# Kernel optimization log

Measured on AMD Instinct MI355X. Metric: run time of the kernel, lower is better.

Reference implementation:

```python
import jax, jax.numpy as jnp
import numpy as np

WEIGHT_MSE = 1.0 / 3.0
W_DNA, W_RNA, W_LIG = 5.0, 5.0, 10.0
EPS = 1e-6


def _weighted_rigid_align(x, x_target, w):
    # x, x_target: [..., N, 3]; w: [..., N]. Aligns x onto x_target (Kabsch).
    w3 = w[..., None]                                   # [..., N, 1]
    wsum = jnp.sum(w, axis=-1, keepdims=True)[..., None]  # [..., 1, 1]
    mu_x = jnp.sum(w3 * x, axis=-2, keepdims=True) / wsum
    mu_t = jnp.sum(w3 * x_target, axis=-2, keepdims=True) / wsum
    xc = x - mu_x
    tc = x_target - mu_t
    # weighted covariance H = sum_n w_n * tc_n tc? -> [..., 3, 3]
    H = jnp.einsum('...ni,...nj->...ij', w3 * tc, xc)
    U, _, Vt = jnp.linalg.svd(H)
    d = jnp.sign(jnp.linalg.det(U @ Vt))                # reflection fix
    D = jnp.stack([jnp.ones_like(d), jnp.ones_like(d), d], axis=-1)
    R = (U * D[..., None, :]) @ Vt                      # [..., 3, 3]
    return jnp.einsum('...ij,...nj->...ni', R, xc) + mu_t


def setup_inputs() -> dict:
    key = jax.random.key(0)
    ks = jax.random.split(key, 7)
    B, S, N = 8, 48, 8192
    pred = jax.random.normal(ks[0], (B, S, N, 3), dtype=jnp.float32)
    true = jax.random.normal(ks[1], (B, N, 3), dtype=jnp.float32)
    mask = jax.random.randint(ks[2], (B, N), 0, 2, dtype=jnp.int32)
    is_dna = jax.random.randint(ks[3], (B, N), 0, 2, dtype=jnp.int32)
    is_rna = jax.random.randint(ks[4], (B, N), 0, 2, dtype=jnp.int32)
    is_lig = jax.random.randint(ks[5], (B, N), 0, 2, dtype=jnp.int32)
    scale = jax.random.uniform(ks[6], (B, S), dtype=jnp.float32)
    return {"pred_coordinate": pred, "true_coordinate": true,
            "coordinate_mask": mask, "is_dna": is_dna, "is_rna": is_rna,
            "is_ligand": is_lig, "per_sample_scale": scale}


def reference(pred_coordinate, true_coordinate, coordinate_mask, is_dna,
              is_rna, is_ligand, per_sample_scale):
    S = pred_coordinate.shape[-3]
    mask = coordinate_mask.astype(jnp.float32)          # [B, N]
    weight = (1.0 + W_DNA * is_dna.astype(jnp.float32)
              + W_RNA * is_rna.astype(jnp.float32)
              + W_LIG * is_ligand.astype(jnp.float32)) * mask
    true_m = true_coordinate * mask[..., None]          # [B, N, 3]
    pred_m = pred_coordinate * mask[..., None, :, None]  # [B, S, N, 3]
    true_e = jnp.broadcast_to(true_m[..., None, :, :], pred_coordinate.shape)
    weight_e = jnp.broadcast_to(weight[..., None, :],
                                pred_coordinate.shape[:-1])  # [B, S, N]
    aligned = jax.lax.stop_gradient(
        _weighted_rigid_align(true_e, pred_m, weight_e))
    weight_e = jax.lax.stop_gradient(weight_e)
    per_atom_se = jnp.sum((pred_coordinate - aligned) ** 2, axis=-1)  # [B,S,N]
    denom = jnp.sum(mask, axis=-1, keepdims=True) + EPS               # [B,1]
    per_sample = jnp.sum(weight_e * per_atom_se, axis=-1) / denom     # [B,S]
    per_sample = per_sample * per_sample_scale
    loss_b = WEIGHT_MSE * jnp.mean(per_sample, axis=-1)               # [B]
    return jnp.mean(loss_b)
```

## Files before the change

### kernel.cpp

```cpp
#include <hip/hip_runtime.h>
#include <math.h>

namespace {

constexpr int NB = 8;
constexpr int NS = 48;
constexpr int NA = 8192;
constexpr int BSIZE = 256;
constexpr int CH = 4;
constexpr int NBS = NB * NS;
constexpr int GRID = CH * NBS;
constexpr int FBS = NBS;

constexpr int PBOFF = NBS * CH * 16;

template <int CNT>
__device__ inline void blockReduceWrite(const float (&v)[CNT], float* __restrict__ dst,
                                        float* lds) {
  const int lane = threadIdx.x & 63;
  const int wave = threadIdx.x >> 6;
#pragma unroll
  for (int k = 0; k < CNT; ++k) {
    float x = v[k];
#pragma unroll
    for (int off = 32; off; off >>= 1) x += __shfl_xor(x, off, 64);
    if (lane == 0) lds[wave * CNT + k] = x;
  }
  __syncthreads();
  if ((int)threadIdx.x < CNT) {
    float s = 0.f;
#pragma unroll
    for (int w = 0; w < BSIZE / 64; ++w) s += lds[w * CNT + threadIdx.x];
    dst[threadIdx.x] = s;
  }
  __syncthreads();
}

__global__ __launch_bounds__(BSIZE) void fused_kernel(
    const float* __restrict__ pred, const float* __restrict__ truec,
    const int* __restrict__ mask, const int* __restrict__ dna,
    const int* __restrict__ rna, const int* __restrict__ lig,
    float* __restrict__ ws) {
  __shared__ float lds[(BSIZE / 64) * 13];
  const int blk = blockIdx.x;
  const int c = blk / NBS;
  const int bs = blk % NBS;
  const int b = bs / NS;
  const bool isS0 = (bs % NS) == 0;

  const float* p = pred + (size_t)bs * NA * 3;
  const float* t = truec + (size_t)b * NA * 3;
  const int mbase = b * NA;

  float acc[13];
#pragma unroll
  for (int k = 0; k < 13; ++k) acc[k] = 0.f;
  float accb[6];
#pragma unroll
  for (int k = 0; k < 6; ++k) accb[k] = 0.f;

  auto atom = [&](float w, float p0, float p1, float p2, float t0, float t1, float t2) {
    const float wp0 = w * p0, wp1 = w * p1, wp2 = w * p2;
    acc[0] += wp0 * p0 + wp1 * p1 + wp2 * p2;
    acc[1] += wp0;
    acc[2] += wp1;
    acc[3] += wp2;
    acc[4] += wp0 * t0;
    acc[5] += wp0 * t1;
    acc[6] += wp0 * t2;
    acc[7] += wp1 * t0;
    acc[8] += wp1 * t1;
    acc[9] += wp1 * t2;
    acc[10] += wp2 * t0;
    acc[11] += wp2 * t1;
    acc[12] += wp2 * t2;
  };
  auto atomb = [&](float mf, float w, float t0, float t1, float t2) {
    accb[0] += w;
    accb[1] += w * t0;
    accb[2] += w * t1;
    accb[3] += w * t2;
    accb[4] += w * (t0 * t0 + t1 * t1 + t2 * t2);
    accb[5] += mf;
  };
  auto wgt = [](int m, int d, int r, int l) {
    return (float)((1 + 5 * (d + r) + 10 * l) * m);
  };

#pragma unroll
  for (int it = 0; it < 2; ++it) {
    const int n0 = c * 2048 + it * 1024 + threadIdx.x * 4;
    const float4 pa = *(const float4*)(p + 3 * n0);
    const float4 pb = *(const float4*)(p + 3 * n0 + 4);
    const float4 pc = *(const float4*)(p + 3 * n0 + 8);
    const float4 ta = *(const float4*)(t + 3 * n0);
    const float4 tb = *(const float4*)(t + 3 * n0 + 4);
    const float4 tc = *(const float4*)(t + 3 * n0 + 8);
    const int4 mk = *(const int4*)(mask + mbase + n0);
    const int4 dn = *(const int4*)(dna + mbase + n0);
    const int4 rn = *(const int4*)(rna + mbase + n0);
    const int4 lg = *(const int4*)(lig + mbase + n0);

    const float w0 = wgt(mk.x, dn.x, rn.x, lg.x);
    const float w1 = wgt(mk.y, dn.y, rn.y, lg.y);
    const float w2 = wgt(mk.z, dn.z, rn.z, lg.z);
    const float w3 = wgt(mk.w, dn.w, rn.w, lg.w);

    atom(w0, pa.x, pa.y, pa.z, ta.x, ta.y, ta.z);
    atom(w1, pa.w, pb.x, pb.y, ta.w, tb.x, tb.y);
    atom(w2, pb.z, pb.w, pc.x, tb.z, tb.w, tc.x);
    atom(w3, pc.y, pc.z, pc.w, tc.y, tc.z, tc.w);

    if (isS0) {
      atomb((float)mk.x, w0, ta.x, ta.y, ta.z);
      atomb((float)mk.y, w1, ta.w, tb.x, tb.y);
      atomb((float)mk.z, w2, tb.z, tb.w, tc.x);
      atomb((float)mk.w, w3, tc.y, tc.z, tc.w);
    }
  }

  blockReduceWrite<13>(acc, ws + (size_t)(bs * CH + c) * 16, lds);
  if (isS0) blockReduceWrite<6>(accb, ws + PBOFF + (size_t)(b * CH + c) * 8, lds);
}

__global__ __launch_bounds__(FBS) void final_kernel(const float* __restrict__ ws,
                                                    const float* __restrict__ scale,
                                                    float* __restrict__ out) {
  const int tid = threadIdx.x;
  __shared__ double bv[NB][6];

  if (tid < NB) {
    double s[6] = {0, 0, 0, 0, 0, 0};
    for (int c = 0; c < CH; ++c) {
      const float* q = ws + PBOFF + (tid * CH + c) * 8;
#pragma unroll
      for (int k = 0; k < 6; ++k) s[k] += (double)q[k];
    }
#pragma unroll
    for (int k = 0; k < 6; ++k) bv[tid][k] = s[k];
  }
  __syncthreads();

  const int b = tid / NS;
  double sums[13];
#pragma unroll
  for (int k = 0; k < 13; ++k) sums[k] = 0.0;
  for (int c = 0; c < CH; ++c) {
    const float4* q4 = (const float4*)(ws + (size_t)(tid * CH + c) * 16);
    const float4 qa = q4[0], qb = q4[1], qc = q4[2], qd = q4[3];
    sums[0] += (double)qa.x;  sums[1] += (double)qa.y;
    sums[2] += (double)qa.z;  sums[3] += (double)qa.w;
    sums[4] += (double)qb.x;  sums[5] += (double)qb.y;
    sums[6] += (double)qb.z;  sums[7] += (double)qb.w;
    sums[8] += (double)qc.x;  sums[9] += (double)qc.y;
    sums[10] += (double)qc.z; sums[11] += (double)qc.w;
    sums[12] += (double)qd.x;
  }

  const double wsum = bv[b][0];
  const double St[3] = {bv[b][1], bv[b][2], bv[b][3]};
  const double stt = bv[b][4];
  const double msum = bv[b][5];

  const double spp = sums[0];
  const double Sp[3] = {sums[1], sums[2], sums[3]};
  const double inv = 1.0 / wsum;

  double H[3][3];
#pragma unroll
  for (int i = 0; i < 3; ++i)
#pragma unroll
    for (int j = 0; j < 3; ++j) H[i][j] = sums[4 + 3 * i + j] - Sp[i] * St[j] * inv;

  const double Sq = spp - (Sp[0] * Sp[0] + Sp[1] * Sp[1] + Sp[2] * Sp[2]) * inv;
  const double Sy = stt - (St[0] * St[0] + St[1] * St[1] + St[2] * St[2]) * inv;

  double K[3][3];
#pragma unroll
  for (int i = 0; i < 3; ++i)
#pragma unroll
    for (int j = 0; j < 3; ++j)
      K[i][j] = H[0][i] * H[0][j] + H[1][i] * H[1][j] + H[2][i] * H[2][j];

  const double q = (K[0][0] + K[1][1] + K[2][2]) / 3.0;
  const double p1 = K[0][1] * K[0][1] + K[0][2] * K[0][2] + K[1][2] * K[1][2];
  const double a0 = K[0][0] - q, a1 = K[1][1] - q, a2 = K[2][2] - q;
  const double p2 = a0 * a0 + a1 * a1 + a2 * a2 + 2.0 * p1;
  double e1, e2, e3;
  if (p2 <= 1e-300) {
    e1 = e2 = e3 = q;
  } else {
    const double pp = sqrt(p2 / 6.0);
    const double ip = 1.0 / pp;
    const double B00 = a0 * ip, B11 = a1 * ip, B22 = a2 * ip;
    const double B01 = K[0][1] * ip, B02 = K[0][2] * ip, B12 = K[1][2] * ip;
    double r = 0.5 * (B00 * (B11 * B22 - B12 * B12) - B01 * (B01 * B22 - B12 * B02) +
                      B02 * (B01 * B12 - B11 * B02));
    float rf = fminf(1.0f, fmaxf(-1.0f, (float)r));
    const float phi = acosf(rf) * (1.0f / 3.0f);
    e1 = q + 2.0 * pp * (double)cosf(phi);
    e3 = q + 2.0 * pp * (double)cosf(phi + 2.0943951023931953f);
    e2 = 3.0 * q - e1 - e3;
  }
  const double s1 = sqrt(fmax(e1, 0.0));
  const double s2 = sqrt(fmax(e2, 0.0));
  const double s3 = sqrt(fmax(e3, 0.0));

  const double detH =
      H[0][0] * (H[1][1] * H[2][2] - H[1][2] * H[2][1]) -
      H[0][1] * (H[1][0] * H[2][2] - H[1][2] * H[2][0]) +
      H[0][2] * (H[1][0] * H[2][1] - H[1][1] * H[2][0]);
  const double d = (detH > 0.0) ? 1.0 : ((detH < 0.0) ? -1.0 : 0.0);

  const double cost = Sq + Sy - 2.0 * (s1 + s2 + d * s3);
  double tot = cost / (msum + 1e-6) * (double)scale[tid];
  tot *= 1.0 / (3.0 * (double)NS * (double)NB);

#pragma unroll
  for (int off = 32; off; off >>= 1) tot += __shfl_xor(tot, off, 64);
  __shared__ double red[FBS / 64];
  if ((tid & 63) == 0) red[tid >> 6] = tot;
  __syncthreads();
  if (tid == 0) {
    double s = 0.0;
#pragma unroll
    for (int w = 0; w < FBS / 64; ++w) s += red[w];
    out[0] = (float)s;
  }
}

}

extern "C" void kernel_launch(void* const* d_in, const int* in_sizes, int n_in,
                              void* d_out, int out_size, void* d_ws, size_t ws_size,
                              hipStream_t stream) {
  const float* pred = (const float*)d_in[0];
  const float* truec = (const float*)d_in[1];
  const int* mask = (const int*)d_in[2];
  const int* dna = (const int*)d_in[3];
  const int* rna = (const int*)d_in[4];
  const int* lig = (const int*)d_in[5];
  const float* scale = (const float*)d_in[6];
  float* ws = (float*)d_ws;
  float* out = (float*)d_out;

  fused_kernel<<<GRID, BSIZE, 0, stream>>>(pred, truec, mask, dna, rna, lig, ws);
  final_kernel<<<1, FBS, 0, stream>>>(ws, scale, out);
}
```

Measured before the change: 25.04 us.

## Fuse partial reduction and Kabsch finalization into one kernel with atomic output

Replaces the two-kernel design (chunked partial sums plus a single-block final kernel) with one kernel where each 512-thread block handles a whole (batch, sample) pair, computes the per-batch true-coordinate statistics itself, solves the 3x3 alignment cost in thread 0, and atomically adds its contribution to the output after a memset. This removes the second launch and the workspace round trip. In exchange it gives up chunk-level parallelism (384 blocks instead of 1536), recomputes the per-batch statistics in every sample block, and makes the final sum depend on float atomic ordering.

Measured after the change: 35.37 us. 41.2% more time.

```diff
diff --git a/kernel.cpp b/kernel.cpp
--- a/kernel.cpp
+++ b/kernel.cpp
@@ -6,48 +6,18 @@
 constexpr int NB = 8;
 constexpr int NS = 48;
 constexpr int NA = 8192;
-constexpr int BSIZE = 256;
-constexpr int CH = 4;
+constexpr int TPB = 512;
 constexpr int NBS = NB * NS;
-constexpr int GRID = CH * NBS;
-constexpr int FBS = NBS;
+constexpr int NW = TPB / 64;
 
-constexpr int PBOFF = NBS * CH * 16;
 
-template <int CNT>
-__device__ inline void blockReduceWrite(const float (&v)[CNT], float* __restrict__ dst,
-                                        float* lds) {
-  const int lane = threadIdx.x & 63;
-  const int wave = threadIdx.x >> 6;
-#pragma unroll
-  for (int k = 0; k < CNT; ++k) {
-    float x = v[k];
-#pragma unroll
-    for (int off = 32; off; off >>= 1) x += __shfl_xor(x, off, 64);
-    if (lane == 0) lds[wave * CNT + k] = x;
-  }
-  __syncthreads();
-  if ((int)threadIdx.x < CNT) {
-    float s = 0.f;
-#pragma unroll
-    for (int w = 0; w < BSIZE / 64; ++w) s += lds[w * CNT + threadIdx.x];
-    dst[threadIdx.x] = s;
-  }
-  __syncthreads();
-}
-
-__global__ __launch_bounds__(BSIZE) void fused_kernel(
+__global__ __launch_bounds__(TPB, 4) void loss_kernel(
     const float* __restrict__ pred, const float* __restrict__ truec,
     const int* __restrict__ mask, const int* __restrict__ dna,
     const int* __restrict__ rna, const int* __restrict__ lig,
-    float* __restrict__ ws) {
-  __shared__ float lds[(BSIZE / 64) * 13];
-  const int blk = blockIdx.x;
-  const int c = blk / NBS;
-  const int bs = blk % NBS;
+    const float* __restrict__ scale, float* __restrict__ out) {
+  const int bs = blockIdx.x;
   const int b = bs / NS;
-  const bool isS0 = (bs % NS) == 0;
-
   const float* p = pred + (size_t)bs * NA * 3;
   const float* t = truec + (size_t)b * NA * 3;
   const int mbase = b * NA;
@@ -59,7 +29,8 @@
 #pragma unroll
   for (int k = 0; k < 6; ++k) accb[k] = 0.f;
 
-  auto atom = [&](float w, float p0, float p1, float p2, float t0, float t1, float t2) {
+  auto atom = [&](float mf, float w, float p0, float p1, float p2, float t0,
+                  float t1, float t2) {
     const float wp0 = w * p0, wp1 = w * p1, wp2 = w * p2;
     acc[0] += wp0 * p0 + wp1 * p1 + wp2 * p2;
     acc[1] += wp0;
@@ -74,8 +45,6 @@
     acc[10] += wp2 * t0;
     acc[11] += wp2 * t1;
     acc[12] += wp2 * t2;
-  };
-  auto atomb = [&](float mf, float w, float t0, float t1, float t2) {
     accb[0] += w;
     accb[1] += w * t0;
     accb[2] += w * t1;
@@ -88,8 +57,8 @@
   };
 
 #pragma unroll
-  for (int it = 0; it < 2; ++it) {
-    const int n0 = c * 2048 + it * 1024 + threadIdx.x * 4;
+  for (int it = 0; it < NA / (TPB * 4); ++it) {
+    const int n0 = it * (TPB * 4) + threadIdx.x * 4;
     const float4 pa = *(const float4*)(p + 3 * n0);
     const float4 pb = *(const float4*)(p + 3 * n0 + 4);
     const float4 pc = *(const float4*)(p + 3 * n0 + 8);
@@ -101,131 +70,93 @@
     const int4 rn = *(const int4*)(rna + mbase + n0);
     const int4 lg = *(const int4*)(lig + mbase + n0);
 
-    const float w0 = wgt(mk.x, dn.x, rn.x, lg.x);
-    const float w1 = wgt(mk.y, dn.y, rn.y, lg.y);
-    const float w2 = wgt(mk.z, dn.z, rn.z, lg.z);
-    const float w3 = wgt(mk.w, dn.w, rn.w, lg.w);
-
-    atom(w0, pa.x, pa.y, pa.z, ta.x, ta.y, ta.z);
-    atom(w1, pa.w, pb.x, pb.y, ta.w, tb.x, tb.y);
-    atom(w2, pb.z, pb.w, pc.x, tb.z, tb.w, tc.x);
-    atom(w3, pc.y, pc.z, pc.w, tc.y, tc.z, tc.w);
-
-    if (isS0) {
-      atomb((float)mk.x, w0, ta.x, ta.y, ta.z);
-      atomb((float)mk.y, w1, ta.w, tb.x, tb.y);
-      atomb((float)mk.z, w2, tb.z, tb.w, tc.x);
-      atomb((float)mk.w, w3, tc.y, tc.z, tc.w);
-    }
+    atom((float)mk.x, wgt(mk.x, dn.x, rn.x, lg.x), pa.x, pa.y, pa.z, ta.x, ta.y, ta.z);
+    atom((float)mk.y, wgt(mk.y, dn.y, rn.y, lg.y), pa.w, pb.x, pb.y, ta.w, tb.x, tb.y);
+    atom((float)mk.z, wgt(mk.z, dn.z, rn.z, lg.z), pb.z, pb.w, pc.x, tb.z, tb.w, tc.x);
+    atom((float)mk.w, wgt(mk.w, dn.w, rn.w, lg.w), pc.y, pc.z, pc.w, tc.y, tc.z, tc.w);
   }
 
-  blockReduceWrite<13>(acc, ws + (size_t)(bs * CH + c) * 16, lds);
-  if (isS0) blockReduceWrite<6>(accb, ws + PBOFF + (size_t)(b * CH + c) * 8, lds);
-}
-
-__global__ __launch_bounds__(FBS) void final_kernel(const float* __restrict__ ws,
-                                                    const float* __restrict__ scale,
-                                                    float* __restrict__ out) {
-  const int tid = threadIdx.x;
-  __shared__ double bv[NB][6];
-
-  if (tid < NB) {
-    double s[6] = {0, 0, 0, 0, 0, 0};
-    for (int c = 0; c < CH; ++c) {
-      const float* q = ws + PBOFF + (tid * CH + c) * 8;
+  __shared__ float lds[NW][19];
+  __shared__ float sums[19];
+  const int lane = threadIdx.x & 63;
+  const int wave = threadIdx.x >> 6;
 #pragma unroll
-      for (int k = 0; k < 6; ++k) s[k] += (double)q[k];
-    }
+  for (int k = 0; k < 19; ++k) {
+    float x = (k < 13) ? acc[k] : accb[k - 13];
 #pragma unroll
-    for (int k = 0; k < 6; ++k) bv[tid][k] = s[k];
+    for (int off = 32; off; off >>= 1) x += __shfl_xor(x, off, 64);
+    if (lane == 0) lds[wave][k] = x;
+  }
+  __syncthreads();
+  if ((int)threadIdx.x < 19) {
+    float s = 0.f;
+#pragma unroll
+    for (int w = 0; w < NW; ++w) s += lds[w][threadIdx.x];
+    sums[threadIdx.x] = s;
   }
   __syncthreads();
 
-  const int b = tid / NS;
-  double sums[13];
+  if (threadIdx.x == 0) {
+    const double wsum = (double)sums[13];
+    const double St[3] = {(double)sums[14], (double)sums[15], (double)sums[16]};
+    const double stt = (double)sums[17];
+    const double msum = (double)sums[18];
+
+    const double spp = (double)sums[0];
+    const double Sp[3] = {(double)sums[1], (double)sums[2], (double)sums[3]};
+    const double inv = 1.0 / wsum;
+
+    double H[3][3];
 #pragma unroll
-  for (int k = 0; k < 13; ++k) sums[k] = 0.0;
-  for (int c = 0; c < CH; ++c) {
-    const float4* q4 = (const float4*)(ws + (size_t)(tid * CH + c) * 16);
-    const float4 qa = q4[0], qb = q4[1], qc = q4[2], qd = q4[3];
-    sums[0] += (double)qa.x;  sums[1] += (double)qa.y;
-    sums[2] += (double)qa.z;  sums[3] += (double)qa.w;
-    sums[4] += (double)qb.x;  sums[5] += (double)qb.y;
-    sums[6] += (double)qb.z;  sums[7] += (double)qb.w;
-    sums[8] += (double)qc.x;  sums[9] += (double)qc.y;
-    sums[10] += (double)qc.z; sums[11] += (double)qc.w;
-    sums[12] += (double)qd.x;
-  }
+    for (int i = 0; i < 3; ++i)
+#pragma unroll
+      for (int j = 0; j < 3; ++j)
+        H[i][j] = (double)sums[4 + 3 * i + j] - Sp[i] * St[j] * inv;
 
-  const double wsum = bv[b][0];
-  const double St[3] = {bv[b][1], bv[b][2], bv[b][3]};
-  const double stt = bv[b][4];
-  const double msum = bv[b][5];
+    const double Sq = spp - (Sp[0] * Sp[0] + Sp[1] * Sp[1] + Sp[2] * Sp[2]) * inv;
+    const double Sy = stt - (St[0] * St[0] + St[1] * St[1] + St[2] * St[2]) * inv;
 
-  const double spp = sums[0];
-  const double Sp[3] = {sums[1], sums[2], sums[3]};
-  const double inv = 1.0 / wsum;
+    double K[3][3];
+#pragma unroll
+    for (int i = 0; i < 3; ++i)
+#pragma unroll
+      for (int j = 0; j < 3; ++j)
+        K[i][j] = H[0][i] * H[0][j] + H[1][i] * H[1][j] + H[2][i] * H[2][j];
 
-  double H[3][3];
-#pragma unroll
-  for (int i = 0; i < 3; ++i)
-#pragma unroll
-    for (int j = 0; j < 3; ++j) H[i][j] = sums[4 + 3 * i + j] - Sp[i] * St[j] * inv;
+    const double q = (K[0][0] + K[1][1] + K[2][2]) / 3.0;
+    const double p1 = K[0][1] * K[0][1] + K[0][2] * K[0][2] + K[1][2] * K[1][2];
+    const double a0 = K[0][0] - q, a1 = K[1][1] - q, a2 = K[2][2] - q;
+    const double p2 = a0 * a0 + a1 * a1 + a2 * a2 + 2.0 * p1;
+    double e1, e2, e3;
+    if (p2 <= 1e-300) {
+      e1 = e2 = e3 = q;
+    } else {
+      const double pp = sqrt(p2 / 6.0);
+      const double ip = 1.0 / pp;
+      const double B00 = a0 * ip, B11 = a1 * ip, B22 = a2 * ip;
+      const double B01 = K[0][1] * ip, B02 = K[0][2] * ip, B12 = K[1][2] * ip;
+      double r = 0.5 * (B00 * (B11 * B22 - B12 * B12) - B01 * (B01 * B22 - B12 * B02) +
+                        B02 * (B01 * B12 - B11 * B02));
+      float rf = fminf(1.0f, fmaxf(-1.0f, (float)r));
+      const float phi = acosf(rf) * (1.0f / 3.0f);
+      e1 = q + 2.0 * pp * (double)cosf(phi);
+      e3 = q + 2.0 * pp * (double)cosf(phi + 2.0943951023931953f);
+      e2 = 3.0 * q - e1 - e3;
+    }
+    const double s1 = sqrt(fmax(e1, 0.0));
+    const double s2 = sqrt(fmax(e2, 0.0));
+    const double s3 = sqrt(fmax(e3, 0.0));
 
-  const double Sq = spp - (Sp[0] * Sp[0] + Sp[1] * Sp[1] + Sp[2] * Sp[2]) * inv;
-  const double Sy = stt - (St[0] * St[0] + St[1] * St[1] + St[2] * St[2]) * inv;
+    const double detH =
+        H[0][0] * (H[1][1] * H[2][2] - H[1][2] * H[2][1]) -
+        H[0][1] * (H[1][0] * H[2][2] - H[1][2] * H[2][0]) +
+        H[0][2] * (H[1][0] * H[2][1] - H[1][1] * H[2][0]);
+    const double d = (detH > 0.0) ? 1.0 : ((detH < 0.0) ? -1.0 : 0.0);
 
-  double K[3][3];
-#pragma unroll
-  for (int i = 0; i < 3; ++i)
-#pragma unroll
-    for (int j = 0; j < 3; ++j)
-      K[i][j] = H[0][i] * H[0][j] + H[1][i] * H[1][j] + H[2][i] * H[2][j];
-
-  const double q = (K[0][0] + K[1][1] + K[2][2]) / 3.0;
-  const double p1 = K[0][1] * K[0][1] + K[0][2] * K[0][2] + K[1][2] * K[1][2];
-  const double a0 = K[0][0] - q, a1 = K[1][1] - q, a2 = K[2][2] - q;
-  const double p2 = a0 * a0 + a1 * a1 + a2 * a2 + 2.0 * p1;
-  double e1, e2, e3;
-  if (p2 <= 1e-300) {
-    e1 = e2 = e3 = q;
-  } else {
-    const double pp = sqrt(p2 / 6.0);
-    const double ip = 1.0 / pp;
-    const double B00 = a0 * ip, B11 = a1 * ip, B22 = a2 * ip;
-    const double B01 = K[0][1] * ip, B02 = K[0][2] * ip, B12 = K[1][2] * ip;
-    double r = 0.5 * (B00 * (B11 * B22 - B12 * B12) - B01 * (B01 * B22 - B12 * B02) +
-                      B02 * (B01 * B12 - B11 * B02));
-    float rf = fminf(1.0f, fmaxf(-1.0f, (float)r));
-    const float phi = acosf(rf) * (1.0f / 3.0f);
-    e1 = q + 2.0 * pp * (double)cosf(phi);
-    e3 = q + 2.0 * pp * (double)cosf(phi + 2.0943951023931953f);
-    e2 = 3.0 * q - e1 - e3;
-  }
-  const double s1 = sqrt(fmax(e1, 0.0));
-  const double s2 = sqrt(fmax(e2, 0.0));
-  const double s3 = sqrt(fmax(e3, 0.0));
-
-  const double detH =
-      H[0][0] * (H[1][1] * H[2][2] - H[1][2] * H[2][1]) -
-      H[0][1] * (H[1][0] * H[2][2] - H[1][2] * H[2][0]) +
-      H[0][2] * (H[1][0] * H[2][1] - H[1][1] * H[2][0]);
-  const double d = (detH > 0.0) ? 1.0 : ((detH < 0.0) ? -1.0 : 0.0);
-
-  const double cost = Sq + Sy - 2.0 * (s1 + s2 + d * s3);
-  double tot = cost / (msum + 1e-6) * (double)scale[tid];
-  tot *= 1.0 / (3.0 * (double)NS * (double)NB);
-
-#pragma unroll
-  for (int off = 32; off; off >>= 1) tot += __shfl_xor(tot, off, 64);
-  __shared__ double red[FBS / 64];
-  if ((tid & 63) == 0) red[tid >> 6] = tot;
-  __syncthreads();
-  if (tid == 0) {
-    double s = 0.0;
-#pragma unroll
-    for (int w = 0; w < FBS / 64; ++w) s += red[w];
-    out[0] = (float)s;
+    const double cost = Sq + Sy - 2.0 * (s1 + s2 + d * s3);
+    const double contrib =
+        cost / (msum + 1e-6) * (double)scale[bs] * (1.0 / (3.0 * (double)NS * (double)NB));
+    atomicAdd(out, (float)contrib);
   }
 }
 
@@ -241,9 +172,8 @@
   const int* rna = (const int*)d_in[4];
   const int* lig = (const int*)d_in[5];
   const float* scale = (const float*)d_in[6];
-  float* ws = (float*)d_ws;
   float* out = (float*)d_out;
 
-  fused_kernel<<<GRID, BSIZE, 0, stream>>>(pred, truec, mask, dna, rna, lig, ws);
-  final_kernel<<<1, FBS, 0, stream>>>(ws, scale, out);
+  hipMemsetAsync(out, 0, sizeof(float), stream);
+  loss_kernel<<<NBS, TPB, 0, stream>>>(pred, truec, mask, dna, rna, lig, scale, out);
 }
```

## Share true-coordinate and weight loads across four samples per block

Applied to the files above, without the earlier changes.

Each block now handles four consecutive samples of one batch over a 2048-atom chunk with 512 threads. It loads true coordinates and the mask, DNA, RNA and ligand flags once and reuses them for all four samples. This cuts redundant reads of the per-batch data and drops the grid from 1536 to 384 blocks. All 58 partial sums are reduced through a single shared-memory pass. In exchange each thread holds 52 accumulators, which raises register pressure, and fewer, larger blocks may reduce latency hiding.

New measurement: 33.80 us. 35.0% more time.

```diff
diff --git a/kernel.cpp b/kernel.cpp
--- a/kernel.cpp
+++ b/kernel.cpp
@@ -6,124 +6,137 @@
 constexpr int NB = 8;
 constexpr int NS = 48;
 constexpr int NA = 8192;
-constexpr int BSIZE = 256;
+constexpr int TPB = 512;
+constexpr int NW = TPB / 64;
 constexpr int CH = 4;
+constexpr int SGRP = 4;
+constexpr int NGRP = NS / SGRP;
 constexpr int NBS = NB * NS;
-constexpr int GRID = CH * NBS;
-constexpr int FBS = NBS;
+constexpr int GRID = NB * CH * NGRP;
 
 constexpr int PBOFF = NBS * CH * 16;
 
-template <int CNT>
-__device__ inline void blockReduceWrite(const float (&v)[CNT], float* __restrict__ dst,
-                                        float* lds) {
-  const int lane = threadIdx.x & 63;
-  const int wave = threadIdx.x >> 6;
-#pragma unroll
-  for (int k = 0; k < CNT; ++k) {
-    float x = v[k];
-#pragma unroll
-    for (int off = 32; off; off >>= 1) x += __shfl_xor(x, off, 64);
-    if (lane == 0) lds[wave * CNT + k] = x;
-  }
-  __syncthreads();
-  if ((int)threadIdx.x < CNT) {
-    float s = 0.f;
-#pragma unroll
-    for (int w = 0; w < BSIZE / 64; ++w) s += lds[w * CNT + threadIdx.x];
-    dst[threadIdx.x] = s;
-  }
-  __syncthreads();
-}
-
-__global__ __launch_bounds__(BSIZE) void fused_kernel(
+__global__ __launch_bounds__(TPB) void stats_kernel(
     const float* __restrict__ pred, const float* __restrict__ truec,
     const int* __restrict__ mask, const int* __restrict__ dna,
     const int* __restrict__ rna, const int* __restrict__ lig,
     float* __restrict__ ws) {
-  __shared__ float lds[(BSIZE / 64) * 13];
   const int blk = blockIdx.x;
-  const int c = blk / NBS;
-  const int bs = blk % NBS;
-  const int b = bs / NS;
-  const bool isS0 = (bs % NS) == 0;
-
-  const float* p = pred + (size_t)bs * NA * 3;
-  const float* t = truec + (size_t)b * NA * 3;
-  const int mbase = b * NA;
-
-  float acc[13];
-#pragma unroll
-  for (int k = 0; k < 13; ++k) acc[k] = 0.f;
-  float accb[6];
-#pragma unroll
-  for (int k = 0; k < 6; ++k) accb[k] = 0.f;
-
-  auto atom = [&](float w, float p0, float p1, float p2, float t0, float t1, float t2) {
-    const float wp0 = w * p0, wp1 = w * p1, wp2 = w * p2;
-    acc[0] += wp0 * p0 + wp1 * p1 + wp2 * p2;
-    acc[1] += wp0;
-    acc[2] += wp1;
-    acc[3] += wp2;
-    acc[4] += wp0 * t0;
-    acc[5] += wp0 * t1;
-    acc[6] += wp0 * t2;
-    acc[7] += wp1 * t0;
-    acc[8] += wp1 * t1;
-    acc[9] += wp1 * t2;
-    acc[10] += wp2 * t0;
-    acc[11] += wp2 * t1;
-    acc[12] += wp2 * t2;
-  };
-  auto atomb = [&](float mf, float w, float t0, float t1, float t2) {
-    accb[0] += w;
-    accb[1] += w * t0;
-    accb[2] += w * t1;
-    accb[3] += w * t2;
-    accb[4] += w * (t0 * t0 + t1 * t1 + t2 * t2);
-    accb[5] += mf;
-  };
+  const int b = blk / (CH * NGRP);
+  const int rem = blk % (CH * NGRP);
+  const int chunk = rem / NGRP;
+  const int sgrp = rem % NGRP;
+  const int bs0 = b * NS + sgrp * SGRP;
+  const bool isG0 = (sgrp == 0);
+
+  const int n0 = chunk * 2048 + threadIdx.x * 4;
+  const int mbase = b * NA + n0;
+  const float* t = truec + ((size_t)b * NA + n0) * 3;
+
+  const float4 ta = *(const float4*)(t);
+  const float4 tb = *(const float4*)(t + 4);
+  const float4 tc = *(const float4*)(t + 8);
+  const int4 mk = *(const int4*)(mask + mbase);
+  const int4 dn = *(const int4*)(dna + mbase);
+  const int4 rn = *(const int4*)(rna + mbase);
+  const int4 lg = *(const int4*)(lig + mbase);
+
   auto wgt = [](int m, int d, int r, int l) {
     return (float)((1 + 5 * (d + r) + 10 * l) * m);
   };
-
-#pragma unroll
-  for (int it = 0; it < 2; ++it) {
-    const int n0 = c * 2048 + it * 1024 + threadIdx.x * 4;
-    const float4 pa = *(const float4*)(p + 3 * n0);
-    const float4 pb = *(const float4*)(p + 3 * n0 + 4);
-    const float4 pc = *(const float4*)(p + 3 * n0 + 8);
-    const float4 ta = *(const float4*)(t + 3 * n0);
-    const float4 tb = *(const float4*)(t + 3 * n0 + 4);
-    const float4 tc = *(const float4*)(t + 3 * n0 + 8);
-    const int4 mk = *(const int4*)(mask + mbase + n0);
-    const int4 dn = *(const int4*)(dna + mbase + n0);
-    const int4 rn = *(const int4*)(rna + mbase + n0);
-    const int4 lg = *(const int4*)(lig + mbase + n0);
-
-    const float w0 = wgt(mk.x, dn.x, rn.x, lg.x);
-    const float w1 = wgt(mk.y, dn.y, rn.y, lg.y);
-    const float w2 = wgt(mk.z, dn.z, rn.z, lg.z);
-    const float w3 = wgt(mk.w, dn.w, rn.w, lg.w);
-
+  const float w0 = wgt(mk.x, dn.x, rn.x, lg.x);
+  const float w1 = wgt(mk.y, dn.y, rn.y, lg.y);
+  const float w2 = wgt(mk.z, dn.z, rn.z, lg.z);
+  const float w3 = wgt(mk.w, dn.w, rn.w, lg.w);
+
+  float acc[SGRP][13];
+#pragma unroll
+  for (int sg = 0; sg < SGRP; ++sg)
+#pragma unroll
+    for (int k = 0; k < 13; ++k) acc[sg][k] = 0.f;
+
+#pragma unroll
+  for (int sg = 0; sg < SGRP; ++sg) {
+    const float* p = pred + ((size_t)(bs0 + sg) * NA + n0) * 3;
+    const float4 pa = *(const float4*)(p);
+    const float4 pb = *(const float4*)(p + 4);
+    const float4 pc = *(const float4*)(p + 8);
+
+    auto atom = [&](float w, float p0, float p1, float p2, float t0, float t1,
+                    float t2) {
+      const float wp0 = w * p0, wp1 = w * p1, wp2 = w * p2;
+      acc[sg][0] += wp0 * p0 + wp1 * p1 + wp2 * p2;
+      acc[sg][1] += wp0;
+      acc[sg][2] += wp1;
+      acc[sg][3] += wp2;
+      acc[sg][4] += wp0 * t0;
+      acc[sg][5] += wp0 * t1;
+      acc[sg][6] += wp0 * t2;
+      acc[sg][7] += wp1 * t0;
+      acc[sg][8] += wp1 * t1;
+      acc[sg][9] += wp1 * t2;
+      acc[sg][10] += wp2 * t0;
+      acc[sg][11] += wp2 * t1;
+      acc[sg][12] += wp2 * t2;
+    };
     atom(w0, pa.x, pa.y, pa.z, ta.x, ta.y, ta.z);
     atom(w1, pa.w, pb.x, pb.y, ta.w, tb.x, tb.y);
     atom(w2, pb.z, pb.w, pc.x, tb.z, tb.w, tc.x);
     atom(w3, pc.y, pc.z, pc.w, tc.y, tc.z, tc.w);
-
-    if (isS0) {
-      atomb((float)mk.x, w0, ta.x, ta.y, ta.z);
-      atomb((float)mk.y, w1, ta.w, tb.x, tb.y);
-      atomb((float)mk.z, w2, tb.z, tb.w, tc.x);
-      atomb((float)mk.w, w3, tc.y, tc.z, tc.w);
-    }
-  }
-
-  blockReduceWrite<13>(acc, ws + (size_t)(bs * CH + c) * 16, lds);
-  if (isS0) blockReduceWrite<6>(accb, ws + PBOFF + (size_t)(b * CH + c) * 8, lds);
-}
-
-__global__ __launch_bounds__(FBS) void final_kernel(const float* __restrict__ ws,
+  }
+
+  float accb[6];
+  if (isG0) {
+    accb[0] = w0 + w1 + w2 + w3;
+    accb[1] = w0 * ta.x + w1 * ta.w + w2 * tb.z + w3 * tc.y;
+    accb[2] = w0 * ta.y + w1 * tb.x + w2 * tb.w + w3 * tc.z;
+    accb[3] = w0 * ta.z + w1 * tb.y + w2 * tc.x + w3 * tc.w;
+    accb[4] = w0 * (ta.x * ta.x + ta.y * ta.y + ta.z * ta.z) +
+              w1 * (ta.w * ta.w + tb.x * tb.x + tb.y * tb.y) +
+              w2 * (tb.z * tb.z + tb.w * tb.w + tc.x * tc.x) +
+              w3 * (tc.y * tc.y + tc.z * tc.z + tc.w * tc.w);
+    accb[5] = (float)(mk.x + mk.y + mk.z + mk.w);
+  }
+
+  __shared__ float lds[NW][58];
+  const int lane = threadIdx.x & 63;
+  const int wave = threadIdx.x >> 6;
+#pragma unroll
+  for (int sg = 0; sg < SGRP; ++sg)
+#pragma unroll
+    for (int k = 0; k < 13; ++k) {
+      float x = acc[sg][k];
+#pragma unroll
+      for (int off = 32; off; off >>= 1) x += __shfl_xor(x, off, 64);
+      if (lane == 0) lds[wave][sg * 13 + k] = x;
+    }
+  if (isG0) {
+#pragma unroll
+    for (int k = 0; k < 6; ++k) {
+      float x = accb[k];
+#pragma unroll
+      for (int off = 32; off; off >>= 1) x += __shfl_xor(x, off, 64);
+      if (lane == 0) lds[wave][52 + k] = x;
+    }
+  }
+  __syncthreads();
+
+  const int nvals = isG0 ? 58 : 52;
+  const int tid = threadIdx.x;
+  if (tid < nvals) {
+    float s = 0.f;
+#pragma unroll
+    for (int w = 0; w < NW; ++w) s += lds[w][tid];
+    if (tid < 52) {
+      const int sg = tid / 13, j = tid % 13;
+      ws[(size_t)((bs0 + sg) * CH + chunk) * 16 + j] = s;
+    } else {
+      ws[PBOFF + (size_t)(b * CH + chunk) * 8 + (tid - 52)] = s;
+    }
+  }
+}
+
+__global__ __launch_bounds__(NBS) void final_kernel(const float* __restrict__ ws,
                                                     const float* __restrict__ scale,
                                                     float* __restrict__ out) {
   const int tid = threadIdx.x;
@@ -218,13 +231,13 @@
 
 #pragma unroll
   for (int off = 32; off; off >>= 1) tot += __shfl_xor(tot, off, 64);
-  __shared__ double red[FBS / 64];
+  __shared__ double red[NBS / 64];
   if ((tid & 63) == 0) red[tid >> 6] = tot;
   __syncthreads();
   if (tid == 0) {
     double s = 0.0;
 #pragma unroll
-    for (int w = 0; w < FBS / 64; ++w) s += red[w];
+    for (int w = 0; w < NBS / 64; ++w) s += red[w];
     out[0] = (float)s;
   }
 }
@@ -244,6 +257,6 @@
   float* ws = (float*)d_ws;
   float* out = (float*)d_out;
 
-  fused_kernel<<<GRID, BSIZE, 0, stream>>>(pred, truec, mask, dna, rna, lig, ws);
-  final_kernel<<<1, FBS, 0, stream>>>(ws, scale, out);
-}
+  stats_kernel<<<GRID, TPB, 0, stream>>>(pred, truec, mask, dna, rna, lig, ws);
+  final_kernel<<<1, NBS, 0, stream>>>(ws, scale, out);
+}
```
